# Kernel optimization log

Measured on AMD Instinct MI355X. Metric: run time of the kernel, lower is better.

The kernel has to match this reference:

```python
import jax, jax.numpy as jnp
import numpy as np

STATE_DIM = 8
SLOT_DIM = 128
B, T, K = 128, 6, 64


def _mlp(x, w1, b1, w2, b2):
    return jax.nn.relu(x @ w1 + b1) @ w2 + b2


def setup_inputs() -> dict:
    key = jax.random.key(0)
    ks = jax.random.split(key, 24)
    s = 0.02
    def w(k, shape):
        return jax.random.normal(k, shape, dtype=jnp.float32) * s
    D, H = STATE_DIM, SLOT_DIM
    return {
        "gt_states": jax.random.normal(ks[0], (B, T, K, D), dtype=jnp.float32),
        "rollout_steps": 5,
        "enc_w1": w(ks[1], (D, H)),  "enc_b1": jnp.zeros((H,), jnp.float32),
        "enc_w2": w(ks[2], (H, H)),  "enc_b2": jnp.zeros((H,), jnp.float32),
        "self_w1": w(ks[3], (H, H)), "self_b1": jnp.zeros((H,), jnp.float32),
        "self_w2": w(ks[4], (H, H)), "self_b2": jnp.zeros((H,), jnp.float32),
        "inter_w1": w(ks[5], (2 * H, H)), "inter_b1": jnp.zeros((H,), jnp.float32),
        "inter_w2": w(ks[6], (H, H)),     "inter_b2": jnp.zeros((H,), jnp.float32),
        "upd_w1": w(ks[7], (2 * H, H)), "upd_b1": jnp.zeros((H,), jnp.float32),
        "upd_w2": w(ks[8], (H, H)),     "upd_b2": jnp.zeros((H,), jnp.float32),
        "dec_w1": w(ks[9], (H, H)),  "dec_b1": jnp.zeros((H,), jnp.float32),
        "dec_w2": w(ks[10], (H, D)), "dec_b2": jnp.zeros((D,), jnp.float32),
    }


def reference(gt_states, rollout_steps, enc_w1, enc_b1, enc_w2, enc_b2,
              self_w1, self_b1, self_w2, self_b2,
              inter_w1, inter_b1, inter_w2, inter_b2,
              upd_w1, upd_b1, upd_w2, upd_b2,
              dec_w1, dec_b1, dec_w2, dec_b2):
    Tn = gt_states.shape[1]
    n_steps = min(Tn - 1, int(rollout_steps))
    H = enc_w1.shape[1]
    # split the concat-MLP first layer: cat([si, sj]) @ W1 == si @ W1a + sj @ W1b
    wi_a, wi_b = inter_w1[:H], inter_w1[H:]

    slots = _mlp(gt_states[:, 0], enc_w1, enc_b1, enc_w2, enc_b2)  # [B,K,H]
    preds = []
    for _ in range(n_steps):
        delta_self = _mlp(slots, self_w1, self_b1, self_w2, self_b2)  # [B,K,H]
        a = slots @ wi_a  # sender (i) contribution, [B,K,H]
        b = slots @ wi_b  # receiver (j) contribution, [B,K,H]
        # pairwise pre-activation [B,K(i),K(j),H]
        pre = a[:, :, None, :] + b[:, None, :, :] + inter_b1
        effects = jax.nn.relu(pre) @ inter_w2 + inter_b2  # [B,K,K,H]
        delta_inter = effects.mean(axis=1)  # mean over i -> [B,K,H]
        slots = _mlp(jnp.concatenate([delta_self, delta_inter], axis=-1),
                     upd_w1, upd_b1, upd_w2, upd_b2)
        pred = _mlp(slots, dec_w1, dec_b1, dec_w2, dec_b2)  # [B,K,D]
        preds.append(pred)
        slots = _mlp(pred, enc_w1, enc_b1, enc_w2, enc_b2)
    pred_states = jnp.stack(preds, axis=1)  # [B,n_steps,K,D]
    target_states = gt_states[:, 1:int(rollout_steps) + 1]
    return pred_states, target_states
```

## Files before the change

### kernel.cpp

```cpp
#include <hip/hip_runtime.h>

#define BB 128
#define TT 6
#define KK 64
#define DD 8
#define HH 128
#define NSTEP 5
#define LDP 136
#define PREDSZ (BB*NSTEP*KK*DD)

typedef unsigned short u16;
typedef unsigned int   u32;
typedef _Float16 f16;
typedef __attribute__((ext_vector_type(8))) _Float16 f16x8;
typedef __attribute__((ext_vector_type(4))) float f32x4;
typedef __attribute__((ext_vector_type(2))) _Float16 h2;

union h2u { u32 u; h2 h; };
union hu  { u16 u; f16 h; };

__device__ __forceinline__ u16 f2h_bits(float f){
  hu v; v.h = (f16)f; return v.u;
}
__device__ __forceinline__ u32 pk2(float x, float y){
  hu a, b; a.h = (f16)x; b.h = (f16)y;
  return (u32)a.u | ((u32)b.u << 16);
}
__device__ __forceinline__ h2 u2h(u32 x){ h2u t; t.u = x; return t.h; }
__device__ __forceinline__ u32 h2u_(h2 x){ h2u t; t.h = x; return t.u; }

#define O_EWA   0
#define O_EWB   16384
#define O_EWS   32768
#define O_SUIU  49152
#define O_UD    81920
#define O_DET   98304
#define O_DW2T  114688
#define BIASF   57856
#define O_XBUF  131072
#define O_FLAG  (O_XBUF + 128*2*2*4096)

template<bool RELU>
__device__ __forceinline__ void gemm16(const u16 (*A)[LDP], const u16* __restrict__ wt,
    float bias, u16 (*O)[LDP], int wn, int wm, int l15, int q, int n, int lane)
{
  f16x8 bf[4];
#pragma unroll
  for (int kc=0; kc<4; ++kc)
    bf[kc] = *(const f16x8*)(wt + (wn<<11) + (kc<<9) + (lane<<3));
  f32x4 acc = {0.f,0.f,0.f,0.f};
#pragma unroll
  for (int kc=0; kc<4; ++kc){
    f16x8 af = *(const f16x8*)&A[(wm<<4)+l15][(kc<<5)+(q<<3)];
    acc = __builtin_amdgcn_mfma_f32_16x16x32_f16(af, bf[kc], acc, 0,0,0);
  }
#pragma unroll
  for (int e=0; e<4; ++e){
    float v = acc[e] + bias;
    if (RELU) v = fmaxf(v, 0.f);
    O[(wm<<4)+(q<<2)+e][n] = f2h_bits(v);
  }
}

__device__ __forceinline__ void gemm256_16(const u16 (*A1)[LDP], const u16 (*A2)[LDP],
    const u16* __restrict__ wt, float bias, u16 (*O)[LDP], int wn, int wm, int l15, int q, int n, int lane)
{
  f16x8 bf[8];
#pragma unroll
  for (int kc=0; kc<8; ++kc)
    bf[kc] = *(const f16x8*)(wt + (wn<<12) + (kc<<9) + (lane<<3));
  f32x4 acc = {0.f,0.f,0.f,0.f};
#pragma unroll
  for (int kc=0; kc<8; ++kc){
    const u16 (*As)[LDP] = (kc<4) ? A1 : A2;
    f16x8 af = *(const f16x8*)&As[(wm<<4)+l15][((kc&3)<<5)+(q<<3)];
    acc = __builtin_amdgcn_mfma_f32_16x16x32_f16(af, bf[kc], acc, 0,0,0);
  }
#pragma unroll
  for (int e=0; e<4; ++e){
    float v = fmaxf(acc[e] + bias, 0.f);
    O[(wm<<4)+(q<<2)+e][n] = f2h_bits(v);
  }
}

__device__ __forceinline__ void fusedS1I(const u16 (*P)[LDP], const u16* __restrict__ ws,
    float bAv, float bBv, float bSv,
    u16 (*Q)[LDP], u16 (*S)[LDP],
    int wn, int wm, int half, int l15, int q, int n, int lane)
{
  const int rowbase = (half<<5) + (wm<<4);
  u32 aPk[4][2];
  {
    f16x8 fa[4];
#pragma unroll
    for (int kc=0; kc<4; ++kc)
      fa[kc] = *(const f16x8*)(ws + O_EWA + (wn<<11) + (kc<<9) + (lane<<3));
#pragma unroll
    for (int mt=0; mt<4; ++mt){
      f32x4 aA = {0.f,0.f,0.f,0.f};
#pragma unroll
      for (int kc=0; kc<4; ++kc){
        f16x8 af = *(const f16x8*)&P[(mt<<4)+l15][(kc<<5)+(q<<3)];
        aA = __builtin_amdgcn_mfma_f32_16x16x32_f16(af, fa[kc], aA, 0,0,0);
      }
      aPk[mt][0] = pk2(aA[0]+bAv, aA[1]+bAv);
      aPk[mt][1] = pk2(aA[2]+bAv, aA[3]+bAv);
    }
  }
  u32 bPk[2];
  {
    f16x8 fb[4], fs[4], af[4];
#pragma unroll
    for (int kc=0; kc<4; ++kc){
      const int o = (wn<<11) + (kc<<9) + (lane<<3);
      fb[kc] = *(const f16x8*)(ws + O_EWB + o);
      fs[kc] = *(const f16x8*)(ws + O_EWS + o);
      af[kc] = *(const f16x8*)&P[rowbase+l15][(kc<<5)+(q<<3)];
    }
    f32x4 aB = {0.f,0.f,0.f,0.f}, aS = {0.f,0.f,0.f,0.f};
#pragma unroll
    for (int kc=0; kc<4; ++kc){
      aB = __builtin_amdgcn_mfma_f32_16x16x32_f16(af[kc], fb[kc], aB, 0,0,0);
      aS = __builtin_amdgcn_mfma_f32_16x16x32_f16(af[kc], fs[kc], aS, 0,0,0);
    }
    bPk[0] = pk2(aB[0]+bBv, aB[1]+bBv);
    bPk[1] = pk2(aB[2]+bBv, aB[3]+bBv);
#pragma unroll
    for (int e=0; e<4; ++e)
      S[(wm<<4)+(q<<2)+e][n] = f2h_bits(fmaxf(aS[e]+bSv, 0.f));
  }

  u32 jt[4][2];
#pragma unroll
  for (int qp=0; qp<4; ++qp){
    const int src = (qp<<4) + l15;
    jt[qp][0] = (u32)__shfl((int)bPk[0], src);
    jt[qp][1] = (u32)__shfl((int)bPk[1], src);
  }
  h2 z; z.x = (f16)0.f; z.y = (f16)0.f;
  h2 s[4][2];
#pragma unroll
  for (int qp=0; qp<4; ++qp){ s[qp][0] = z; s[qp][1] = z; }
#pragma unroll
  for (int mt=0; mt<4; ++mt)
#pragma unroll
    for (int pp=0; pp<2; ++pp){
      const u32 ap = aPk[mt][pp];
      const h2 hl = u2h(__builtin_amdgcn_perm(ap, ap, 0x01000100));
      const h2 hh = u2h(__builtin_amdgcn_perm(ap, ap, 0x03020302));
#pragma unroll
      for (int qp=0; qp<4; ++qp)
#pragma unroll
        for (int p=0; p<2; ++p){
          const h2 bt = u2h(jt[qp][p]);
          s[qp][p] += __builtin_elementwise_max(hl + bt, z);
          s[qp][p] += __builtin_elementwise_max(hh + bt, z);
        }
    }
#pragma unroll
  for (int m=0; m<2; ++m){
    const int msk = 16 << m;
#pragma unroll
    for (int qp=0; qp<4; ++qp)
#pragma unroll
      for (int p=0; p<2; ++p)
        s[qp][p] += u2h((u32)__shfl_xor((int)h2u_(s[qp][p]), msk));
  }
#pragma unroll
  for (int qp=0; qp<4; ++qp) if (qp == q){
#pragma unroll
    for (int p=0; p<2; ++p){
      const int j = (wm<<4) + (qp<<2) + (p<<1);
      hu lo, hi; lo.h = s[qp][p].x; hi.h = s[qp][p].y;
      Q[j][n]   = lo.u;
      Q[j+1][n] = hi.u;
    }
  }
}

__device__ __forceinline__ void dec_out(const u16 (*S)[LDP], const u16* __restrict__ dwt,
    float db2v, float* __restrict__ out, int batch, int half, int t, int tid)
{
  const int r = tid>>3, d = tid&7;
  float acc = db2v;
#pragma unroll
  for (int c=0; c<16; ++c){
    f16x8 hv = *(const f16x8*)&S[r][c<<3];
    f16x8 wv = *(const f16x8*)(dwt + (d<<7) + (c<<3));
#pragma unroll
    for (int j=0; j<8; ++j)
      acc += (float)hv[j] * (float)wv[j];
  }
  out[(size_t)(batch*NSTEP + t)*(KK*DD) + ((half<<5)+r)*DD + d] = acc;
}

__device__ __forceinline__ void mlp_in8(const float* pred, const float* __restrict__ W,
    const float* __restrict__ bias, u16 (*O)[LDP], int tid)
{
  const int h = tid & 127, rg = tid >> 7;
  float wv[DD];
#pragma unroll
  for (int d=0; d<DD; ++d) wv[d] = W[d*HH + h];
  const float bv = bias[h];
  for (int rr=0; rr<8; ++rr){
    const int r = (rg<<3) + rr;
    float v = bv;
#pragma unroll
    for (int d=0; d<DD; ++d) v += pred[r*DD + d] * wv[d];
    O[r][h] = f2h_bits(fmaxf(v, 0.f));
  }
}

__global__ void prep_kernel(
    const float* __restrict__ ew1, const float* __restrict__ eb1,
    const float* __restrict__ ew2, const float* __restrict__ eb2,
    const float* __restrict__ sw1, const float* __restrict__ sb1,
    const float* __restrict__ sw2, const float* __restrict__ sb2,
    const float* __restrict__ iw1, const float* __restrict__ ib1,
    const float* __restrict__ iw2, const float* __restrict__ ib2,
    const float* __restrict__ uw1, const float* __restrict__ ub1,
    const float* __restrict__ uw2, const float* __restrict__ ub2,
    const float* __restrict__ dw1, const float* __restrict__ db1,
    const float* __restrict__ dw2, const float* __restrict__ db2,
    u16* __restrict__ ws)
{
  const int idx = blockIdx.x * 256 + threadIdx.x;
  if (idx < 512) ((u32*)(ws + O_FLAG))[idx] = 0;
  if (idx < 49152){
    const int mat = idx >> 14, r = idx & 16383;
    const int g = r >> 11, kc = (r >> 9) & 3, lane = (r >> 3) & 63, e = r & 7;
    const int k  = (kc<<5) + ((lane>>4)<<3) + e;
    const int nn = (g<<4) + (lane & 15);
    float v = 0.f;
    if (mat == 0){ for (int m=0; m<HH; ++m) v += ew2[k*HH+m] * iw1[m*HH+nn]; }
    else if (mat == 1){ for (int m=0; m<HH; ++m) v += ew2[k*HH+m] * iw1[(HH+m)*HH+nn]; }
    else { for (int m=0; m<HH; ++m) v += ew2[k*HH+m] * sw1[m*HH+nn]; }
    hu hb; hb.h = (f16)v; ws[idx] = hb.u;
  } else if (idx < 81920){
    const int r = idx - 49152;
    const int g = r >> 12, kc = (r >> 9) & 7, lane = (r >> 3) & 63, e = r & 7;
    const int k  = ((kc&3)<<5) + ((lane>>4)<<3) + e;
    const int nn = (g<<4) + (lane & 15);
    float v = 0.f;
    if (kc < 4){ for (int m=0; m<HH; ++m) v += sw2[k*HH+m] * uw1[m*HH+nn]; }
    else { for (int m=0; m<HH; ++m) v += iw2[k*HH+m] * uw1[(HH+m)*HH+nn]; v *= (1.f/64.f); }
    hu hb; hb.h = (f16)v; ws[idx] = hb.u;
  } else if (idx < 98304){
    const int r = idx - 81920;
    const int g = r >> 11, kc = (r >> 9) & 3, lane = (r >> 3) & 63, e = r & 7;
    const int k  = (kc<<5) + ((lane>>4)<<3) + e;
    const int nn = (g<<4) + (lane & 15);
    float v = 0.f;
    for (int m=0; m<HH; ++m) v += uw2[k*HH+m] * dw1[m*HH+nn];
    hu hb; hb.h = (f16)v; ws[idx] = hb.u;
  } else if (idx < 114688){
    const int r = idx - 98304;
    const int g = r >> 11, kc = (r >> 9) & 3, lane = (r >> 3) & 63, e = r & 7;
    const int k  = (kc<<5) + ((lane>>4)<<3) + e;
    const int nn = (g<<4) + (lane & 15);
    float v = 0.f;
#pragma unroll
    for (int d=0; d<DD; ++d) v += dw2[k*DD+d] * ew1[d*HH+nn];
    hu hb; hb.h = (f16)v; ws[idx] = hb.u;
  } else if (idx < 115712){
    const int r = idx - 114688, d = r >> 7, hcol = r & 127;
    hu hb; hb.h = (f16)dw2[hcol*DD + d]; ws[idx] = hb.u;
  } else if (idx < 116480){
    const int j = idx - 115712, which = j >> 7, nn = j & 127;
    float v = 0.f;
    switch (which){
      case 0: for (int m=0; m<HH; ++m) v += eb2[m] * iw1[m*HH+nn]; break;
      case 1: for (int m=0; m<HH; ++m) v += eb2[m] * iw1[(HH+m)*HH+nn]; v += ib1[nn]; break;
      case 2: for (int m=0; m<HH; ++m) v += eb2[m] * sw1[m*HH+nn]; v += sb1[nn]; break;
      case 3: for (int m=0; m<HH; ++m) v += sb2[m]*uw1[m*HH+nn] + ib2[m]*uw1[(HH+m)*HH+nn];
              v += ub1[nn]; break;
      case 4: for (int m=0; m<HH; ++m) v += ub2[m] * dw1[m*HH+nn]; v += db1[nn]; break;
      default:
#pragma unroll
        for (int d=0; d<DD; ++d) v += db2[d] * ew1[d*HH+nn];
        v += eb1[nn]; break;
    }
    ((float*)ws)[BIASF + j] = v;
  }
}

__global__ __launch_bounds__(1024, 1) void rollout_kernel(
    const float* __restrict__ gt, const int* __restrict__ rollout,
    const float* __restrict__ ew1, const float* __restrict__ eb1,
    const float* __restrict__ db2,
    u16* __restrict__ ws, float* __restrict__ out)
{
  extern __shared__ u16 smem[];
  u16 (*P)[LDP] = (u16(*)[LDP])smem;
  u16 (*Q)[LDP] = (u16(*)[LDP])(smem + 64*LDP);
  u16 (*R)[LDP] = (u16(*)[LDP])(smem + 96*LDP);
  u16 (*S)[LDP] = (u16(*)[LDP])(smem + 128*LDP);
  float* predbuf = (float*)Q;

  const int tid = threadIdx.x, blk = blockIdx.x;
  const int batch = blk & 127, half = blk >> 7;
  const int w = tid >> 6, lane = tid & 63;
  const int l15 = lane & 15, q = lane >> 4;
  const int wn = w & 7, wm = w >> 3;
  const int n = (wn << 4) + l15;

  int ns = rollout[0];
  if (ns > TT-1) ns = TT-1;
  if (ns > NSTEP) ns = NSTEP;
  if (ns < 0) ns = 0;

  const float* bf32 = (const float*)ws;
  const float bAv  = bf32[BIASF + n];
  const float bBv  = bf32[BIASF + 128 + n];
  const float bSv  = bf32[BIASF + 256 + n];
  const float bUv  = bf32[BIASF + 384 + n];
  const float bUDv = bf32[BIASF + 512 + n];
  const float debv = bf32[BIASF + 640 + n];
  const float db2v = db2[tid & 7];

  u16* xbuf  = ws + O_XBUF;
  u32* flags = (u32*)(ws + O_FLAG);
  const int own  = (batch<<1) + half;
  const int prt  = (batch<<1) + (1-half);

  for (int i = tid; i < (NSTEP*KK*DD/2); i += 1024)
    out[PREDSZ + batch*(NSTEP*KK*DD) + half*(NSTEP*KK*DD/2) + i]
      = gt[(size_t)batch*(TT*KK*DD) + KK*DD + half*(NSTEP*KK*DD/2) + i];
  if (tid < KK*DD) predbuf[tid] = gt[(size_t)batch*(TT*KK*DD) + tid];
  __syncthreads();
  mlp_in8(predbuf, ew1, eb1, P, tid);
  __syncthreads();

  for (int t=0; t<ns; ++t){
    fusedS1I(P, ws, bAv, bBv, bSv, Q, S, wn, wm, half, l15, q, n, lane);
    __syncthreads();
    gemm256_16(S, Q, ws+O_SUIU, bUv, R, wn, wm, l15, q, n, lane);
    __syncthreads();
    gemm16<true>(R, ws+O_UD, bUDv, S, wn, wm, l15, q, n, lane);
    __syncthreads();
    {
      f16x8 bfw[4];
#pragma unroll
      for (int kc=0; kc<4; ++kc)
        bfw[kc] = *(const f16x8*)(ws + O_DET + (wn<<11) + (kc<<9) + (lane<<3));
      f32x4 acc = {0.f,0.f,0.f,0.f};
#pragma unroll
      for (int kc=0; kc<4; ++kc){
        f16x8 af = *(const f16x8*)&S[(wm<<4)+l15][(kc<<5)+(q<<3)];
        acc = __builtin_amdgcn_mfma_f32_16x16x32_f16(af, bfw[kc], acc, 0,0,0);
      }
      const int par = t & 1;
      u16* ob = xbuf + (((own<<1)|par)<<12);
      const bool exch = (t < ns-1);
#pragma unroll
      for (int e=0; e<4; ++e){
        const u16 bits = f2h_bits(fmaxf(acc[e]+debv, 0.f));
        const int lr = (wm<<4)+(q<<2)+e;
        P[(half<<5)+lr][n] = bits;
        if (exch) ob[(lr<<7) | n] = bits;
      }
    }
    if (tid < 256) dec_out(S, ws+O_DW2T, db2v, out, batch, half, t, tid);
    __syncthreads();

    if (t < ns-1){
      const int par = t & 1;
      if (tid == 0){
        __hip_atomic_store(&flags[(own<<1)|par], (u32)(t+1),
                           __ATOMIC_RELEASE, __HIP_MEMORY_SCOPE_AGENT);
        int guard = 0;
        while (__hip_atomic_load(&flags[(prt<<1)|par],
                 __ATOMIC_ACQUIRE, __HIP_MEMORY_SCOPE_AGENT) != (u32)(t+1)
               && guard < (1<<22)){
          ++guard;
          __builtin_amdgcn_s_sleep(1);
        }
      }
      __syncthreads();
      if (tid < 512){
        const u16* pb = xbuf + (((prt<<1)|par)<<12);
        const int r = tid >> 4, c = (tid & 15) << 3;
        *(f16x8*)&P[((1-half)<<5)+r][c] = *(const f16x8*)(pb + (r<<7) + c);
      }
      __syncthreads();
    }
  }
}

extern "C" void kernel_launch(void* const* d_in, const int* in_sizes, int n_in,
                              void* d_out, int out_size, void* d_ws, size_t ws_size,
                              hipStream_t stream)
{
  const float* gt  = (const float*)d_in[0];
  const int*   rs  = (const int*)d_in[1];
  const float* ew1 = (const float*)d_in[2];
  const float* eb1 = (const float*)d_in[3];
  const float* ew2 = (const float*)d_in[4];
  const float* eb2 = (const float*)d_in[5];
  const float* sw1 = (const float*)d_in[6];
  const float* sb1 = (const float*)d_in[7];
  const float* sw2 = (const float*)d_in[8];
  const float* sb2 = (const float*)d_in[9];
  const float* iw1 = (const float*)d_in[10];
  const float* ib1 = (const float*)d_in[11];
  const float* iw2 = (const float*)d_in[12];
  const float* ib2 = (const float*)d_in[13];
  const float* uw1 = (const float*)d_in[14];
  const float* ub1 = (const float*)d_in[15];
  const float* uw2 = (const float*)d_in[16];
  const float* ub2 = (const float*)d_in[17];
  const float* dw1 = (const float*)d_in[18];
  const float* db1 = (const float*)d_in[19];
  const float* dw2 = (const float*)d_in[20];
  const float* db2 = (const float*)d_in[21];
  float* out = (float*)d_out;
  u16*   ws  = (u16*)d_ws;

  const int smem_bytes = 160 * LDP * (int)sizeof(u16);
  (void)hipFuncSetAttribute((const void*)rollout_kernel,
                            hipFuncAttributeMaxDynamicSharedMemorySize, smem_bytes);

  hipLaunchKernelGGL(prep_kernel, dim3(455), dim3(256), 0, stream,
                     ew1, eb1, ew2, eb2, sw1, sb1, sw2, sb2, iw1, ib1, iw2, ib2,
                     uw1, ub1, uw2, ub2, dw1, db1, dw2, db2, ws);
  hipLaunchKernelGGL(rollout_kernel, dim3(2*BB), dim3(1024), smem_bytes, stream,
                     gt, rs, ew1, eb1, db2, ws, out);
}
```

Baseline: 186.5 us.

## Read partner half's slots directly from global exchange buffer with per-wave flag waits

Each block now keeps only its own 32 slot rows in shared memory and reads the partner block's rows straight from the global exchange buffer inside the fused interaction stage. The wait on the partner flag moves to the start of each step and is done per wave, which removes the two extra block barriers and the copy into shared memory. The initial encoder is also split so each half encodes only its own rows and publishes them. This cuts shared memory and synchronisation on the critical path. The cost is global-memory latency in the fused stage and a more delicate flag and parity protocol.

```diff
diff --git a/kernel.cpp b/kernel.cpp
--- a/kernel.cpp
+++ b/kernel.cpp
@@ -83,29 +83,35 @@
   }
 }
 
-__device__ __forceinline__ void fusedS1I(const u16 (*P)[LDP], const u16* __restrict__ ws,
+__device__ __forceinline__ void fusedS1I(const u16 (*P)[LDP], const u16* __restrict__ xprt,
+    const u16* __restrict__ ws,
     float bAv, float bBv, float bSv,
     u16 (*Q)[LDP], u16 (*S)[LDP],
     int wn, int wm, int half, int l15, int q, int n, int lane)
 {
-  const int rowbase = (half<<5) + (wm<<4);
+  f16x8 fa[4];
+#pragma unroll
+  for (int kc=0; kc<4; ++kc)
+    fa[kc] = *(const f16x8*)(ws + O_EWA + (wn<<11) + (kc<<9) + (lane<<3));
+  f16x8 afx[2][4];
+#pragma unroll
+  for (int u=0; u<2; ++u)
+#pragma unroll
+    for (int kc=0; kc<4; ++kc)
+      afx[u][kc] = *(const f16x8*)(xprt + ((((u<<4)+l15)<<7) | ((kc<<5)+(q<<3))));
+
   u32 aPk[4][2];
-  {
-    f16x8 fa[4];
-#pragma unroll
-    for (int kc=0; kc<4; ++kc)
-      fa[kc] = *(const f16x8*)(ws + O_EWA + (wn<<11) + (kc<<9) + (lane<<3));
-#pragma unroll
-    for (int mt=0; mt<4; ++mt){
-      f32x4 aA = {0.f,0.f,0.f,0.f};
-#pragma unroll
-      for (int kc=0; kc<4; ++kc){
-        f16x8 af = *(const f16x8*)&P[(mt<<4)+l15][(kc<<5)+(q<<3)];
-        aA = __builtin_amdgcn_mfma_f32_16x16x32_f16(af, fa[kc], aA, 0,0,0);
-      }
-      aPk[mt][0] = pk2(aA[0]+bAv, aA[1]+bAv);
-      aPk[mt][1] = pk2(aA[2]+bAv, aA[3]+bAv);
-    }
+#pragma unroll
+  for (int u=0; u<2; ++u){
+    const int mt = (half<<1) + u;
+    f32x4 aA = {0.f,0.f,0.f,0.f};
+#pragma unroll
+    for (int kc=0; kc<4; ++kc){
+      f16x8 af = *(const f16x8*)&P[(u<<4)+l15][(kc<<5)+(q<<3)];
+      aA = __builtin_amdgcn_mfma_f32_16x16x32_f16(af, fa[kc], aA, 0,0,0);
+    }
+    aPk[mt][0] = pk2(aA[0]+bAv, aA[1]+bAv);
+    aPk[mt][1] = pk2(aA[2]+bAv, aA[3]+bAv);
   }
   u32 bPk[2];
   {
@@ -115,7 +121,7 @@
       const int o = (wn<<11) + (kc<<9) + (lane<<3);
       fb[kc] = *(const f16x8*)(ws + O_EWB + o);
       fs[kc] = *(const f16x8*)(ws + O_EWS + o);
-      af[kc] = *(const f16x8*)&P[rowbase+l15][(kc<<5)+(q<<3)];
+      af[kc] = *(const f16x8*)&P[(wm<<4)+l15][(kc<<5)+(q<<3)];
     }
     f32x4 aB = {0.f,0.f,0.f,0.f}, aS = {0.f,0.f,0.f,0.f};
 #pragma unroll
@@ -128,6 +134,16 @@
 #pragma unroll
     for (int e=0; e<4; ++e)
       S[(wm<<4)+(q<<2)+e][n] = f2h_bits(fmaxf(aS[e]+bSv, 0.f));
+  }
+#pragma unroll
+  for (int u=0; u<2; ++u){
+    const int mt = ((1-half)<<1) + u;
+    f32x4 aA = {0.f,0.f,0.f,0.f};
+#pragma unroll
+    for (int kc=0; kc<4; ++kc)
+      aA = __builtin_amdgcn_mfma_f32_16x16x32_f16(afx[u][kc], fa[kc], aA, 0,0,0);
+    aPk[mt][0] = pk2(aA[0]+bAv, aA[1]+bAv);
+    aPk[mt][1] = pk2(aA[2]+bAv, aA[3]+bAv);
   }
 
   u32 jt[4][2];
@@ -192,23 +208,6 @@
       acc += (float)hv[j] * (float)wv[j];
   }
   out[(size_t)(batch*NSTEP + t)*(KK*DD) + ((half<<5)+r)*DD + d] = acc;
-}
-
-__device__ __forceinline__ void mlp_in8(const float* pred, const float* __restrict__ W,
-    const float* __restrict__ bias, u16 (*O)[LDP], int tid)
-{
-  const int h = tid & 127, rg = tid >> 7;
-  float wv[DD];
-#pragma unroll
-  for (int d=0; d<DD; ++d) wv[d] = W[d*HH + h];
-  const float bv = bias[h];
-  for (int rr=0; rr<8; ++rr){
-    const int r = (rg<<3) + rr;
-    float v = bv;
-#pragma unroll
-    for (int d=0; d<DD; ++d) v += pred[r*DD + d] * wv[d];
-    O[r][h] = f2h_bits(fmaxf(v, 0.f));
-  }
 }
 
 __global__ void prep_kernel(
@@ -292,9 +291,9 @@
 {
   extern __shared__ u16 smem[];
   u16 (*P)[LDP] = (u16(*)[LDP])smem;
-  u16 (*Q)[LDP] = (u16(*)[LDP])(smem + 64*LDP);
-  u16 (*R)[LDP] = (u16(*)[LDP])(smem + 96*LDP);
-  u16 (*S)[LDP] = (u16(*)[LDP])(smem + 128*LDP);
+  u16 (*Q)[LDP] = (u16(*)[LDP])(smem + 32*LDP);
+  u16 (*R)[LDP] = (u16(*)[LDP])(smem + 64*LDP);
+  u16 (*S)[LDP] = (u16(*)[LDP])(smem + 96*LDP);
   float* predbuf = (float*)Q;
 
   const int tid = threadIdx.x, blk = blockIdx.x;
@@ -326,13 +325,46 @@
   for (int i = tid; i < (NSTEP*KK*DD/2); i += 1024)
     out[PREDSZ + batch*(NSTEP*KK*DD) + half*(NSTEP*KK*DD/2) + i]
       = gt[(size_t)batch*(TT*KK*DD) + KK*DD + half*(NSTEP*KK*DD/2) + i];
-  if (tid < KK*DD) predbuf[tid] = gt[(size_t)batch*(TT*KK*DD) + tid];
+  if (tid < 256) predbuf[tid] = gt[(size_t)batch*(TT*KK*DD) + (half<<8) + tid];
   __syncthreads();
-  mlp_in8(predbuf, ew1, eb1, P, tid);
+  {
+    const int h = tid & 127, rg = tid >> 7;
+    float wv[DD];
+#pragma unroll
+    for (int d=0; d<DD; ++d) wv[d] = ew1[d*HH + h];
+    const float bv = eb1[h];
+    u16* ob0 = xbuf + (((own<<1)|0)<<12);
+    for (int rr=0; rr<4; ++rr){
+      const int lr = (rg<<2) + rr;
+      float v = bv;
+#pragma unroll
+      for (int d=0; d<DD; ++d) v += predbuf[lr*DD + d] * wv[d];
+      const u16 bits = f2h_bits(fmaxf(v, 0.f));
+      P[lr][h] = bits;
+      ob0[(lr<<7) | h] = bits;
+    }
+  }
   __syncthreads();
+  if (tid == 0)
+    __hip_atomic_store(&flags[(own<<1)|0], 1u, __ATOMIC_RELEASE, __HIP_MEMORY_SCOPE_AGENT);
 
   for (int t=0; t<ns; ++t){
-    fusedS1I(P, ws, bAv, bBv, bSv, Q, S, wn, wm, half, l15, q, n, lane);
+    {
+      const u32 tag = (u32)(t+1);
+      if (lane == 0){
+        int guard = 0;
+        while (__hip_atomic_load(&flags[(prt<<1)|(t&1)],
+                 __ATOMIC_RELAXED, __HIP_MEMORY_SCOPE_AGENT) != tag
+               && guard < (1<<22)){
+          ++guard;
+          __builtin_amdgcn_s_sleep(1);
+        }
+      }
+      __builtin_amdgcn_fence(__ATOMIC_ACQUIRE, "agent");
+    }
+    const u16* xprt = xbuf + (((prt<<1)|(t&1))<<12);
+
+    fusedS1I(P, xprt, ws, bAv, bBv, bSv, Q, S, wn, wm, half, l15, q, n, lane);
     __syncthreads();
     gemm256_16(S, Q, ws+O_SUIU, bUv, R, wn, wm, l15, q, n, lane);
     __syncthreads();
@@ -349,41 +381,21 @@
         f16x8 af = *(const f16x8*)&S[(wm<<4)+l15][(kc<<5)+(q<<3)];
         acc = __builtin_amdgcn_mfma_f32_16x16x32_f16(af, bfw[kc], acc, 0,0,0);
       }
-      const int par = t & 1;
-      u16* ob = xbuf + (((own<<1)|par)<<12);
+      u16* ob = xbuf + (((own<<1)|((t+1)&1))<<12);
       const bool exch = (t < ns-1);
 #pragma unroll
       for (int e=0; e<4; ++e){
         const u16 bits = f2h_bits(fmaxf(acc[e]+debv, 0.f));
         const int lr = (wm<<4)+(q<<2)+e;
-        P[(half<<5)+lr][n] = bits;
+        P[lr][n] = bits;
         if (exch) ob[(lr<<7) | n] = bits;
       }
     }
     if (tid < 256) dec_out(S, ws+O_DW2T, db2v, out, batch, half, t, tid);
     __syncthreads();
-
-    if (t < ns-1){
-      const int par = t & 1;
-      if (tid == 0){
-        __hip_atomic_store(&flags[(own<<1)|par], (u32)(t+1),
-                           __ATOMIC_RELEASE, __HIP_MEMORY_SCOPE_AGENT);
-        int guard = 0;
-        while (__hip_atomic_load(&flags[(prt<<1)|par],
-                 __ATOMIC_ACQUIRE, __HIP_MEMORY_SCOPE_AGENT) != (u32)(t+1)
-               && guard < (1<<22)){
-          ++guard;
-          __builtin_amdgcn_s_sleep(1);
-        }
-      }
-      __syncthreads();
-      if (tid < 512){
-        const u16* pb = xbuf + (((prt<<1)|par)<<12);
-        const int r = tid >> 4, c = (tid & 15) << 3;
-        *(f16x8*)&P[((1-half)<<5)+r][c] = *(const f16x8*)(pb + (r<<7) + c);
-      }
-      __syncthreads();
-    }
+    if (t < ns-1 && tid == 0)
+      __hip_atomic_store(&flags[(own<<1)|((t+1)&1)], (u32)(t+2),
+                         __ATOMIC_RELEASE, __HIP_MEMORY_SCOPE_AGENT);
   }
 }
 
@@ -416,7 +428,7 @@
   float* out = (float*)d_out;
   u16*   ws  = (u16*)d_ws;
 
-  const int smem_bytes = 160 * LDP * (int)sizeof(u16);
+  const int smem_bytes = 128 * LDP * (int)sizeof(u16);
   (void)hipFuncSetAttribute((const void*)rollout_kernel,
                             hipFuncAttributeMaxDynamicSharedMemorySize, smem_bytes);
 
```

Measured after the change: 339.8 us. 82.3% more time.
